# Performance work log

Hardware: AMD Instinct MI355X
Metric: run time of the kernel (lower is better)

The kernel has to match this reference:

```python
import jax, jax.numpy as jnp
import numpy as np
import math

D_MODEL = 1024
NUM_HEADS = 16
HEAD_DIM = D_MODEL // NUM_HEADS


def _sinusoidal_pe(seq_len, dim, dtype=jnp.float32):
    # Matches RotaryPositionEmbedding buffer: pe[:,0::2]=sin, pe[:,1::2]=cos
    pos = jnp.arange(seq_len, dtype=jnp.float32)[:, None]            # [S,1]
    div = jnp.exp(jnp.arange(0, dim, 2, dtype=jnp.float32) * (-math.log(10000.0) / dim))  # [dim/2]
    ang = pos * div[None, :]                                          # [S,dim/2]
    pe = jnp.stack([jnp.sin(ang), jnp.cos(ang)], axis=-1).reshape(seq_len, dim)
    return pe.astype(dtype)


def setup_inputs() -> dict:
    key = jax.random.key(0)
    ks = jax.random.split(key, 11)
    B, S, D = 4, 1024, D_MODEL
    s = 1.0 / math.sqrt(D)
    inp = {
        "q": jax.random.normal(ks[0], (B, S, D), jnp.float32),
        "k": jax.random.normal(ks[1], (B, S, D), jnp.float32),
        "v": jax.random.normal(ks[2], (B, S, D), jnp.float32),
        "Wq": jax.random.normal(ks[3], (D, D), jnp.float32) * s,
        "bq": jax.random.normal(ks[4], (D,), jnp.float32) * s,
        "Wk": jax.random.normal(ks[5], (D, D), jnp.float32) * s,
        "bk": jax.random.normal(ks[6], (D,), jnp.float32) * s,
        "Wv": jax.random.normal(ks[7], (D, D), jnp.float32) * s,
        "bv": jax.random.normal(ks[8], (D,), jnp.float32) * s,
        "Wo": jax.random.normal(ks[9], (D, D), jnp.float32) * s,
        "bo": jax.random.normal(ks[10], (D,), jnp.float32) * s,
    }
    return inp


def reference(q, k, v, Wq, bq, Wk, bk, Wv, bv, Wo, bo):
    B, S, D = q.shape
    H, hd = NUM_HEADS, HEAD_DIM
    scale = hd ** -0.5

    def proj(x, W, b):  # nn.Linear: x @ W.T + b, then [B,H,S,hd]
        return (x @ W.T + b).reshape(B, S, H, hd).transpose(0, 2, 1, 3)

    qh = proj(q, Wq, bq)
    kh = proj(k, Wk, bk)
    vh = proj(v, Wv, bv)

    pe = _sinusoidal_pe(S, hd, qh.dtype)[None, None]  # [1,1,S,hd]
    qh = qh + pe
    kh = kh + pe

    scores = jnp.einsum("bhqd,bhkd->bhqk", qh, kh) * scale  # [B,H,S,S]
    attn = jax.nn.softmax(scores, axis=-1)
    out = jnp.einsum("bhqk,bhkd->bhqd", attn, vh)            # [B,H,S,hd]
    out = out.transpose(0, 2, 1, 3).reshape(B, S, D)
    return out @ Wo.T + bo
```

## Files before the change

kernel.cpp:

```cpp
#include <hip/hip_runtime.h>
#include <hip/hip_bf16.h>

#define B_  4
#define S_  1024
#define D_  1024
#define H_  16
#define HD_ 64

typedef __bf16 bf16;
typedef __bf16 bf16x8 __attribute__((ext_vector_type(8)));
typedef __bf16 bf16x4 __attribute__((ext_vector_type(4)));
typedef float  f32x4  __attribute__((ext_vector_type(4)));

__device__ __forceinline__ void gll16(const void* g, void* l) {
    __builtin_amdgcn_global_load_lds((__attribute__((address_space(1))) void*)(void*)g,
                                     (__attribute__((address_space(3))) void*)l,
                                     16, 0, 0);
}

__global__ __launch_bounds__(256)
void convert_w_kernel(const float* __restrict__ Wq, const float* __restrict__ Wk,
                      const float* __restrict__ Wv, const float* __restrict__ Wo,
                      bf16* __restrict__ dst)
{
    const int idx   = blockIdx.x * 256 + threadIdx.x;
    const int which = idx >> 17;
    const int off   = (idx & 131071) * 8;
    const float* s  = (which == 0) ? Wq : (which == 1) ? Wk : (which == 2) ? Wv : Wo;
    const f32x4 a = *(const f32x4*)(s + off);
    const f32x4 b = *(const f32x4*)(s + off + 4);
    bf16x8 o;
#pragma unroll
    for (int jj = 0; jj < 4; ++jj) { o[jj] = (bf16)a[jj]; o[jj + 4] = (bf16)b[jj]; }
    *(bf16x8*)(dst + ((size_t)which << 20) + off) = o;
}

__global__ __launch_bounds__(256)
void qkv_proj_kernel(const float* __restrict__ qin, const float* __restrict__ kin,
                     const float* __restrict__ vin,
                     const bf16* __restrict__ Wall,
                     const float* __restrict__ bq, const float* __restrict__ bk,
                     const float* __restrict__ bv,
                     bf16* __restrict__ Qh, bf16* __restrict__ Kh,
                     bf16* __restrict__ Vt)
{
    __shared__ __align__(16) bf16 sA[128 * 32];
    __shared__ __align__(16) bf16 sB[128 * 32];

    const int z = blockIdx.z;
    const float* __restrict__ X    = (z == 0) ? qin : (z == 1) ? kin : vin;
    const float* __restrict__ bias = (z == 0) ? bq  : (z == 1) ? bk  : bv;

    const int m0   = blockIdx.y * 128;
    const int n0   = blockIdx.x * 128;
    const int tid  = threadIdx.x;
    const int lane = tid & 63;
    const int wave = tid >> 6;
    const int lr   = lane & 15;
    const int lg   = lane >> 4;
    const int mw   = (wave >> 1) * 64;
    const int nw   = (wave & 1) * 64;
    const int srow = tid >> 2;
    const int skg  = (tid & 3) * 8;

    f32x4 acc[4][4];
#pragma unroll
    for (int i = 0; i < 4; ++i)
#pragma unroll
        for (int j = 0; j < 4; ++j) acc[i][j] = (f32x4){0.f, 0.f, 0.f, 0.f};

    const float* Ab = X + (size_t)(m0 + srow) * D_ + skg;
    const bf16*  Wb = Wall + ((size_t)z << 20) + (size_t)(n0 + srow) * D_ + skg;

    for (int kt = 0; kt < 32; ++kt) {
        const int k0 = kt * 32;
        f32x4 ga[2][2];
#pragma unroll
        for (int p = 0; p < 2; ++p) {
            const float* ar = Ab + (size_t)(p * 64) * D_ + k0;
            ga[p][0] = *(const f32x4*)(ar);
            ga[p][1] = *(const f32x4*)(ar + 4);
        }
        __syncthreads();
#pragma unroll
        for (int p = 0; p < 2; ++p)
            gll16(Wb + (size_t)(p * 64) * D_ + k0, (char*)sB + p * 4096 + tid * 16);
#pragma unroll
        for (int p = 0; p < 2; ++p) {
            bf16x8 ta;
#pragma unroll
            for (int jj = 0; jj < 4; ++jj) {
                ta[jj]     = (bf16)ga[p][0][jj];
                ta[jj + 4] = (bf16)ga[p][1][jj];
            }
            *(bf16x8*)(sA + p * 2048 + tid * 8) = ta;
        }
        __syncthreads();

        bf16x8 af[4], bfr[4];
#pragma unroll
        for (int i = 0; i < 4; ++i)
            af[i] = *(const bf16x8*)(sA + (mw + 16 * i + lr) * 32 + lg * 8);
#pragma unroll
        for (int j = 0; j < 4; ++j)
            bfr[j] = *(const bf16x8*)(sB + (nw + 16 * j + lr) * 32 + lg * 8);
#pragma unroll
        for (int i = 0; i < 4; ++i)
#pragma unroll
            for (int j = 0; j < 4; ++j)
                acc[i][j] = __builtin_amdgcn_mfma_f32_16x16x32_bf16(af[i], bfr[j],
                                                                    acc[i][j], 0, 0, 0);
    }

    if (z < 2) {
        bf16* dst = (z == 0) ? Qh : Kh;
#pragma unroll
        for (int i = 0; i < 4; ++i) {
#pragma unroll
            for (int j = 0; j < 4; ++j) {
                const int n = n0 + nw + 16 * j + lr;
                const int h = n >> 6, d = n & 63;
                const float bn = bias[n];
                const float dv_rev = 0.15915494309189535f *
                    exp2f(-(float)(d & ~1) * 0.20762050593046648f);
#pragma unroll
                for (int r = 0; r < 4; ++r) {
                    const int m = m0 + mw + 16 * i + lg * 4 + r;
                    const int b = m >> 10, s = m & 1023;
                    float rev = (float)s * dv_rev;
                    rev -= floorf(rev);
                    const float sv = __builtin_amdgcn_sinf(rev);
                    const float cv = __builtin_amdgcn_cosf(rev);
                    const float pe  = (d & 1) ? cv : sv;
                    const float val = acc[i][j][r] + bn + pe;
                    dst[(size_t)((b * H_ + h) * S_ + s) * HD_ + d] = (bf16)val;
                }
            }
        }
    } else {
#pragma unroll
        for (int i = 0; i < 4; ++i) {
            const int mb = m0 + mw + 16 * i + lg * 4;
            const int b = mb >> 10, sb = mb & 1023;
#pragma unroll
            for (int j = 0; j < 4; ++j) {
                const int n = n0 + nw + 16 * j + lr;
                const int h = n >> 6, d = n & 63;
                const float bn = bias[n];
                bf16x4 pk;
#pragma unroll
                for (int r = 0; r < 4; ++r) pk[r] = (bf16)(acc[i][j][r] + bn);
                *(bf16x4*)(Vt + (size_t)((b * H_ + h) * HD_ + d) * S_ + sb) = pk;
            }
        }
    }
}

#define LDK 72
__global__ __launch_bounds__(128)
void attn_kernel(const bf16* __restrict__ Qh, const bf16* __restrict__ Kh,
                 const bf16* __restrict__ Vt, bf16* __restrict__ att)
{
    __shared__ __align__(16) bf16 sK[64 * LDK];
    __shared__ __align__(16) bf16 sV[64 * LDK];
    __shared__ __align__(16) bf16 sP[2 * 32 * LDK];

    const int tid  = threadIdx.x;
    const int lane = tid & 63;
    const int wave = tid >> 6;
    const int lr   = lane & 15;
    const int lg   = lane >> 4;
    const int bh   = blockIdx.y;
    const int qw   = blockIdx.x * 64 + wave * 32;

    const bf16* Qb = Qh + (size_t)bh * S_ * HD_;
    const bf16* Kb = Kh + (size_t)bh * S_ * HD_;
    const bf16* Vb = Vt + (size_t)bh * HD_ * S_;

    bf16x8 qa[2][2];
#pragma unroll
    for (int i = 0; i < 2; ++i)
#pragma unroll
        for (int ks = 0; ks < 2; ++ks)
            qa[i][ks] = *(const bf16x8*)(Qb + (size_t)(qw + 16 * i + lr) * HD_ +
                                         ks * 32 + lg * 8);

    f32x4 o[2][4];
    float lsum[2][4];
#pragma unroll
    for (int i = 0; i < 2; ++i) {
#pragma unroll
        for (int jd = 0; jd < 4; ++jd) o[i][jd] = (f32x4){0.f, 0.f, 0.f, 0.f};
#pragma unroll
        for (int r = 0; r < 4; ++r) lsum[i][r] = 0.f;
    }

    bf16* const pw   = sP + wave * 32 * LDK;
    const int  srow  = tid >> 3;
    const int  scol  = (tid & 7) * 8;

    for (int kc = 0; kc < 16; ++kc) {
        bf16x8 kv[4], vv[4];
#pragma unroll
        for (int p = 0; p < 4; ++p) {
            kv[p] = *(const bf16x8*)(Kb + (size_t)(kc * 64 + p * 16 + srow) * HD_ + scol);
            vv[p] = *(const bf16x8*)(Vb + (size_t)(p * 16 + srow) * S_ + kc * 64 + scol);
        }
        __syncthreads();
#pragma unroll
        for (int p = 0; p < 4; ++p) {
            *(bf16x8*)(sK + (p * 16 + srow) * LDK + scol) = kv[p];
            *(bf16x8*)(sV + (p * 16 + srow) * LDK + scol) = vv[p];
        }
        __syncthreads();

        bf16x8 kb[4][2];
#pragma unroll
        for (int jk = 0; jk < 4; ++jk)
#pragma unroll
            for (int ks = 0; ks < 2; ++ks)
                kb[jk][ks] = *(const bf16x8*)(sK + (16 * jk + lr) * LDK + ks * 32 + lg * 8);

#pragma unroll
        for (int i = 0; i < 2; ++i)
#pragma unroll
            for (int jk = 0; jk < 4; ++jk) {
                f32x4 s = (f32x4){0.f, 0.f, 0.f, 0.f};
                s = __builtin_amdgcn_mfma_f32_16x16x32_bf16(qa[i][0], kb[jk][0], s, 0, 0, 0);
                s = __builtin_amdgcn_mfma_f32_16x16x32_bf16(qa[i][1], kb[jk][1], s, 0, 0, 0);
#pragma unroll
                for (int r = 0; r < 4; ++r) {
                    const float pp = __expf(s[r] * 0.125f);
                    lsum[i][r] += pp;
                    pw[(16 * i + lg * 4 + r) * LDK + 16 * jk + lr] = (bf16)pp;
                }
            }
        asm volatile("s_waitcnt lgkmcnt(0)" ::: "memory");

#pragma unroll
        for (int ks = 0; ks < 2; ++ks) {
            bf16x8 pa[2];
#pragma unroll
            for (int i = 0; i < 2; ++i)
                pa[i] = *(const bf16x8*)(pw + (16 * i + lr) * LDK + ks * 32 + lg * 8);
#pragma unroll
            for (int jd = 0; jd < 4; ++jd) {
                const bf16x8 vb = *(const bf16x8*)(sV + (16 * jd + lr) * LDK +
                                                   ks * 32 + lg * 8);
#pragma unroll
                for (int i = 0; i < 2; ++i)
                    o[i][jd] = __builtin_amdgcn_mfma_f32_16x16x32_bf16(pa[i], vb,
                                                                       o[i][jd], 0, 0, 0);
            }
        }
    }

    const int b = bh >> 4, h = bh & 15;
#pragma unroll
    for (int i = 0; i < 2; ++i)
#pragma unroll
        for (int r = 0; r < 4; ++r) {
            float l = lsum[i][r];
#pragma unroll
            for (int off = 1; off < 16; off <<= 1)
                l += __shfl_xor(l, off, 64);
            const float inv = 1.f / l;
            const int s = qw + 16 * i + lg * 4 + r;
#pragma unroll
            for (int jd = 0; jd < 4; ++jd) {
                const int d = 16 * jd + lr;
                att[(size_t)(b * S_ + s) * D_ + h * HD_ + d] = (bf16)(o[i][jd][r] * inv);
            }
        }
}

__global__ __launch_bounds__(256)
void out_proj_kernel(const bf16* __restrict__ A, const bf16* __restrict__ Wob,
                     const float* __restrict__ bo, float* __restrict__ out)
{
    __shared__ __align__(16) bf16 sA[128 * 32];
    __shared__ __align__(16) bf16 sB[128 * 32];

    const int m0   = blockIdx.y * 128;
    const int n0   = blockIdx.x * 128;
    const int tid  = threadIdx.x;
    const int lane = tid & 63;
    const int wave = tid >> 6;
    const int lr   = lane & 15;
    const int lg   = lane >> 4;
    const int mw   = (wave >> 1) * 64;
    const int nw   = (wave & 1) * 64;
    const int srow = tid >> 2;
    const int skg  = (tid & 3) * 8;

    f32x4 acc[4][4];
#pragma unroll
    for (int i = 0; i < 4; ++i)
#pragma unroll
        for (int j = 0; j < 4; ++j) acc[i][j] = (f32x4){0.f, 0.f, 0.f, 0.f};

    const bf16* Ab = A   + (size_t)(m0 + srow) * D_ + skg;
    const bf16* Wb = Wob + (size_t)(n0 + srow) * D_ + skg;

    for (int kt = 0; kt < 32; ++kt) {
        const int k0 = kt * 32;
        __syncthreads();
#pragma unroll
        for (int p = 0; p < 2; ++p) {
            gll16(Ab + (size_t)(p * 64) * D_ + k0, (char*)sA + p * 4096 + tid * 16);
            gll16(Wb + (size_t)(p * 64) * D_ + k0, (char*)sB + p * 4096 + tid * 16);
        }
        __syncthreads();

        bf16x8 af[4], bfr[4];
#pragma unroll
        for (int i = 0; i < 4; ++i)
            af[i] = *(const bf16x8*)(sA + (mw + 16 * i + lr) * 32 + lg * 8);
#pragma unroll
        for (int j = 0; j < 4; ++j)
            bfr[j] = *(const bf16x8*)(sB + (nw + 16 * j + lr) * 32 + lg * 8);
#pragma unroll
        for (int i = 0; i < 4; ++i)
#pragma unroll
            for (int j = 0; j < 4; ++j)
                acc[i][j] = __builtin_amdgcn_mfma_f32_16x16x32_bf16(af[i], bfr[j],
                                                                    acc[i][j], 0, 0, 0);
    }

#pragma unroll
    for (int i = 0; i < 4; ++i)
#pragma unroll
        for (int j = 0; j < 4; ++j) {
            const int n = n0 + nw + 16 * j + lr;
            const float bn = bo[n];
#pragma unroll
            for (int r = 0; r < 4; ++r) {
                const int m = m0 + mw + 16 * i + lg * 4 + r;
                out[(size_t)m * D_ + n] = acc[i][j][r] + bn;
            }
        }
}

extern "C" void kernel_launch(void* const* d_in, const int* in_sizes, int n_in,
                              void* d_out, int out_size, void* d_ws, size_t ws_size,
                              hipStream_t stream)
{
    const float* q  = (const float*)d_in[0];
    const float* k  = (const float*)d_in[1];
    const float* v  = (const float*)d_in[2];
    const float* Wq = (const float*)d_in[3];
    const float* bq = (const float*)d_in[4];
    const float* Wk = (const float*)d_in[5];
    const float* bk = (const float*)d_in[6];
    const float* Wv = (const float*)d_in[7];
    const float* bv = (const float*)d_in[8];
    const float* Wo = (const float*)d_in[9];
    const float* bo = (const float*)d_in[10];

    char* ws = (char*)d_ws;
    const size_t SZ = (size_t)B_ * H_ * S_ * HD_ * sizeof(bf16);
    bf16* Qh  = (bf16*)(ws);
    bf16* Kh  = (bf16*)(ws + SZ);
    bf16* Vt  = (bf16*)(ws + 2 * SZ);
    bf16* att = (bf16*)(ws + 3 * SZ);

    bf16* Wall = (bf16*)d_out;

    convert_w_kernel<<<2048, 256, 0, stream>>>(Wq, Wk, Wv, Wo, Wall);
    qkv_proj_kernel<<<dim3(8, 32, 3), 256, 0, stream>>>(q, k, v, Wall, bq, bk, bv,
                                                        Qh, Kh, Vt);
    attn_kernel<<<dim3(16, 64), 128, 0, stream>>>(Qh, Kh, Vt, att);
    hipMemcpyAsync((void*)Qh, (const void*)(Wall + ((size_t)3 << 20)),
                   (size_t)D_ * D_ * sizeof(bf16), hipMemcpyDeviceToDevice, stream);
    out_proj_kernel<<<dim3(8, 32), 256, 0, stream>>>(att, (const bf16*)Qh, bo,
                                                     (float*)d_out);
}
```

Baseline: 233.1 us.

## Pre-convert activations to bf16 and use async LDS loads in QKV GEMM

When the workspace is large enough, one kernel converts the q/k/v activations and all four weight matrices to bf16 in scratch. The QKV projection then streams pure bf16 tiles into LDS with global_load_lds instead of converting fp32 on the fly, and the device-to-device memcpy of Wo is dropped. Grids are flattened to 1D with the m index varying fastest, so consecutive blocks share weight tiles in cache. The cost is an extra full read and write pass over the activations, and the old path is kept as a fallback for small workspaces.

```diff
diff --git a/kernel.cpp b/kernel.cpp
--- a/kernel.cpp
+++ b/kernel.cpp
@@ -16,6 +16,36 @@
     __builtin_amdgcn_global_load_lds((__attribute__((address_space(1))) void*)(void*)g,
                                      (__attribute__((address_space(3))) void*)l,
                                      16, 0, 0);
+}
+
+__global__ __launch_bounds__(256)
+void convert_all_kernel(const float* __restrict__ q, const float* __restrict__ k,
+                        const float* __restrict__ v,
+                        const float* __restrict__ Wq, const float* __restrict__ Wk,
+                        const float* __restrict__ Wv, const float* __restrict__ Wo,
+                        bf16* __restrict__ Xb, bf16* __restrict__ Wall)
+{
+    const size_t e = ((size_t)blockIdx.x * 256 + threadIdx.x) * 8;
+    const size_t M4 = (size_t)1 << 22;
+    const float* s;
+    bf16* d;
+    if (e < 3 * M4) {
+        const int which = (int)(e >> 22);
+        s = ((which == 0) ? q : (which == 1) ? k : v) + (e - ((size_t)which << 22));
+        d = Xb + e;
+    } else {
+        const size_t r = e - 3 * M4;
+        const int which = (int)(r >> 20);
+        s = ((which == 0) ? Wq : (which == 1) ? Wk : (which == 2) ? Wv : Wo) +
+            (r - ((size_t)which << 20));
+        d = Wall + r;
+    }
+    const f32x4 a = *(const f32x4*)s;
+    const f32x4 b = *(const f32x4*)(s + 4);
+    bf16x8 o;
+#pragma unroll
+    for (int jj = 0; jj < 4; ++jj) { o[jj] = (bf16)a[jj]; o[jj + 4] = (bf16)b[jj]; }
+    *(bf16x8*)d = o;
 }
 
 __global__ __launch_bounds__(256)
@@ -35,14 +65,130 @@
     *(bf16x8*)(dst + ((size_t)which << 20) + off) = o;
 }
 
+__device__ __forceinline__ void qkv_epilogue(
+    f32x4 (&acc)[4][4], int z, int m0, int n0, int mw, int nw, int lr, int lg,
+    const float* __restrict__ bias,
+    bf16* __restrict__ Qh, bf16* __restrict__ Kh, bf16* __restrict__ Vt)
+{
+    if (z < 2) {
+        bf16* dst = (z == 0) ? Qh : Kh;
+#pragma unroll
+        for (int i = 0; i < 4; ++i) {
+#pragma unroll
+            for (int j = 0; j < 4; ++j) {
+                const int n = n0 + nw + 16 * j + lr;
+                const int h = n >> 6, d = n & 63;
+                const float bn = bias[n];
+                const float dv_rev = 0.15915494309189535f *
+                    exp2f(-(float)(d & ~1) * 0.20762050593046648f);
+#pragma unroll
+                for (int r = 0; r < 4; ++r) {
+                    const int m = m0 + mw + 16 * i + lg * 4 + r;
+                    const int b = m >> 10, s = m & 1023;
+                    float rev = (float)s * dv_rev;
+                    rev -= floorf(rev);
+                    const float sv = __builtin_amdgcn_sinf(rev);
+                    const float cv = __builtin_amdgcn_cosf(rev);
+                    const float pe  = (d & 1) ? cv : sv;
+                    const float val = acc[i][j][r] + bn + pe;
+                    dst[(size_t)((b * H_ + h) * S_ + s) * HD_ + d] = (bf16)val;
+                }
+            }
+        }
+    } else {
+#pragma unroll
+        for (int i = 0; i < 4; ++i) {
+            const int mb = m0 + mw + 16 * i + lg * 4;
+            const int b = mb >> 10, sb = mb & 1023;
+#pragma unroll
+            for (int j = 0; j < 4; ++j) {
+                const int n = n0 + nw + 16 * j + lr;
+                const int h = n >> 6, d = n & 63;
+                const float bn = bias[n];
+                bf16x4 pk;
+#pragma unroll
+                for (int r = 0; r < 4; ++r) pk[r] = (bf16)(acc[i][j][r] + bn);
+                *(bf16x4*)(Vt + (size_t)((b * H_ + h) * HD_ + d) * S_ + sb) = pk;
+            }
+        }
+    }
+}
+
 __global__ __launch_bounds__(256)
-void qkv_proj_kernel(const float* __restrict__ qin, const float* __restrict__ kin,
-                     const float* __restrict__ vin,
-                     const bf16* __restrict__ Wall,
-                     const float* __restrict__ bq, const float* __restrict__ bk,
-                     const float* __restrict__ bv,
-                     bf16* __restrict__ Qh, bf16* __restrict__ Kh,
-                     bf16* __restrict__ Vt)
+void qkv_proj_bf16_kernel(const bf16* __restrict__ Xb, const bf16* __restrict__ Wall,
+                          const float* __restrict__ bq, const float* __restrict__ bk,
+                          const float* __restrict__ bv,
+                          bf16* __restrict__ Qh, bf16* __restrict__ Kh,
+                          bf16* __restrict__ Vt)
+{
+    __shared__ __align__(16) bf16 sA[128 * 32];
+    __shared__ __align__(16) bf16 sB[128 * 32];
+
+    const int blk  = blockIdx.x;
+    const int mIdx = blk & 31;
+    const int t    = blk >> 5;
+    const int nIdx = t & 7;
+    const int z    = t >> 3;
+
+    const int m0 = mIdx * 128, n0 = nIdx * 128;
+    const bf16* __restrict__ X = Xb + ((size_t)z << 22);
+    const bf16* __restrict__ W = Wall + ((size_t)z << 20);
+    const float* __restrict__ bias = (z == 0) ? bq : (z == 1) ? bk : bv;
+
+    const int tid  = threadIdx.x;
+    const int lane = tid & 63;
+    const int wave = tid >> 6;
+    const int lr   = lane & 15;
+    const int lg   = lane >> 4;
+    const int mw   = (wave >> 1) * 64;
+    const int nw   = (wave & 1) * 64;
+    const int srow = tid >> 2;
+    const int skg  = (tid & 3) * 8;
+
+    f32x4 acc[4][4];
+#pragma unroll
+    for (int i = 0; i < 4; ++i)
+#pragma unroll
+        for (int j = 0; j < 4; ++j) acc[i][j] = (f32x4){0.f, 0.f, 0.f, 0.f};
+
+    const bf16* Ab = X + (size_t)(m0 + srow) * D_ + skg;
+    const bf16* Wb = W + (size_t)(n0 + srow) * D_ + skg;
+
+    for (int kt = 0; kt < 32; ++kt) {
+        const int k0 = kt * 32;
+        __syncthreads();
+#pragma unroll
+        for (int p = 0; p < 2; ++p) {
+            gll16(Ab + (size_t)(p * 64) * D_ + k0, (char*)sA + p * 4096 + tid * 16);
+            gll16(Wb + (size_t)(p * 64) * D_ + k0, (char*)sB + p * 4096 + tid * 16);
+        }
+        __syncthreads();
+
+        bf16x8 af[4], bfr[4];
+#pragma unroll
+        for (int i = 0; i < 4; ++i)
+            af[i] = *(const bf16x8*)(sA + (mw + 16 * i + lr) * 32 + lg * 8);
+#pragma unroll
+        for (int j = 0; j < 4; ++j)
+            bfr[j] = *(const bf16x8*)(sB + (nw + 16 * j + lr) * 32 + lg * 8);
+#pragma unroll
+        for (int i = 0; i < 4; ++i)
+#pragma unroll
+            for (int j = 0; j < 4; ++j)
+                acc[i][j] = __builtin_amdgcn_mfma_f32_16x16x32_bf16(af[i], bfr[j],
+                                                                    acc[i][j], 0, 0, 0);
+    }
+    qkv_epilogue(acc, z, m0, n0, mw, nw, lr, lg, bias, Qh, Kh, Vt);
+}
+
+__global__ __launch_bounds__(256)
+void qkv_proj_mixed_kernel(const float* __restrict__ qin, const float* __restrict__ kin,
+                           const float* __restrict__ vin,
+                           const bf16* __restrict__ Wall,
+                           const float* __restrict__ bq, const float* __restrict__ bk,
+                           const float* __restrict__ bv,
+                           bf16* __restrict__ Qh, bf16* __restrict__ Kh,
+                           bf16* __restrict__ Vt)
 {
     __shared__ __align__(16) bf16 sA[128 * 32];
     __shared__ __align__(16) bf16 sB[128 * 32];
@@ -111,49 +257,7 @@
                 acc[i][j] = __builtin_amdgcn_mfma_f32_16x16x32_bf16(af[i], bfr[j],
                                                                     acc[i][j], 0, 0, 0);
     }
-
-    if (z < 2) {
-        bf16* dst = (z == 0) ? Qh : Kh;
-#pragma unroll
-        for (int i = 0; i < 4; ++i) {
-#pragma unroll
-            for (int j = 0; j < 4; ++j) {
-                const int n = n0 + nw + 16 * j + lr;
-                const int h = n >> 6, d = n & 63;
-                const float bn = bias[n];
-                const float dv_rev = 0.15915494309189535f *
-                    exp2f(-(float)(d & ~1) * 0.20762050593046648f);
-#pragma unroll
-                for (int r = 0; r < 4; ++r) {
-                    const int m = m0 + mw + 16 * i + lg * 4 + r;
-                    const int b = m >> 10, s = m & 1023;
-                    float rev = (float)s * dv_rev;
-                    rev -= floorf(rev);
-                    const float sv = __builtin_amdgcn_sinf(rev);
-                    const float cv = __builtin_amdgcn_cosf(rev);
-                    const float pe  = (d & 1) ? cv : sv;
-                    const float val = acc[i][j][r] + bn + pe;
-                    dst[(size_t)((b * H_ + h) * S_ + s) * HD_ + d] = (bf16)val;
-                }
-            }
-        }
-    } else {
-#pragma unroll
-        for (int i = 0; i < 4; ++i) {
-            const int mb = m0 + mw + 16 * i + lg * 4;
-            const int b = mb >> 10, sb = mb & 1023;
-#pragma unroll
-            for (int j = 0; j < 4; ++j) {
-                const int n = n0 + nw + 16 * j + lr;
-                const int h = n >> 6, d = n & 63;
-                const float bn = bias[n];
-                bf16x4 pk;
-#pragma unroll
-                for (int r = 0; r < 4; ++r) pk[r] = (bf16)(acc[i][j][r] + bn);
-                *(bf16x4*)(Vt + (size_t)((b * H_ + h) * HD_ + d) * S_ + sb) = pk;
-            }
-        }
-    }
+    qkv_epilogue(acc, z, m0, n0, mw, nw, lr, lg, bias, Qh, Kh, Vt);
 }
 
 #define LDK 72
@@ -170,8 +274,9 @@
     const int wave = tid >> 6;
     const int lr   = lane & 15;
     const int lg   = lane >> 4;
-    const int bh   = blockIdx.y;
-    const int qw   = blockIdx.x * 64 + wave * 32;
+    const int bh   = blockIdx.x & 63;
+    const int qt   = blockIdx.x >> 6;
+    const int qw   = qt * 64 + wave * 32;
 
     const bf16* Qb = Qh + (size_t)bh * S_ * HD_;
     const bf16* Kb = Kh + (size_t)bh * S_ * HD_;
@@ -281,8 +386,11 @@
     __shared__ __align__(16) bf16 sA[128 * 32];
     __shared__ __align__(16) bf16 sB[128 * 32];
 
-    const int m0   = blockIdx.y * 128;
-    const int n0   = blockIdx.x * 128;
+    const int blk  = blockIdx.x;
+    const int mIdx = blk & 31;
+    const int nIdx = blk >> 5;
+    const int m0 = mIdx * 128, n0 = nIdx * 128;
+
     const int tid  = threadIdx.x;
     const int lane = tid & 63;
     const int wave = tid >> 6;
@@ -358,20 +466,32 @@
     const float* bo = (const float*)d_in[10];
 
     char* ws = (char*)d_ws;
-    const size_t SZ = (size_t)B_ * H_ * S_ * HD_ * sizeof(bf16);
+    const size_t MB8 = (size_t)8 * 1024 * 1024;
     bf16* Qh  = (bf16*)(ws);
-    bf16* Kh  = (bf16*)(ws + SZ);
-    bf16* Vt  = (bf16*)(ws + 2 * SZ);
-    bf16* att = (bf16*)(ws + 3 * SZ);
-
-    bf16* Wall = (bf16*)d_out;
-
-    convert_w_kernel<<<2048, 256, 0, stream>>>(Wq, Wk, Wv, Wo, Wall);
-    qkv_proj_kernel<<<dim3(8, 32, 3), 256, 0, stream>>>(q, k, v, Wall, bq, bk, bv,
-                                                        Qh, Kh, Vt);
-    attn_kernel<<<dim3(16, 64), 128, 0, stream>>>(Qh, Kh, Vt, att);
-    hipMemcpyAsync((void*)Qh, (const void*)(Wall + ((size_t)3 << 20)),
-                   (size_t)D_ * D_ * sizeof(bf16), hipMemcpyDeviceToDevice, stream);
-    out_proj_kernel<<<dim3(8, 32), 256, 0, stream>>>(att, (const bf16*)Qh, bo,
-                                                     (float*)d_out);
-}
+    bf16* Kh  = (bf16*)(ws + MB8);
+    bf16* Vt  = (bf16*)(ws + 2 * MB8);
+    bf16* att = (bf16*)(ws + 3 * MB8);
+
+    if (ws_size >= (size_t)64 * 1024 * 1024) {
+        bf16* Xb   = (bf16*)(ws + 4 * MB8);
+        bf16* Wall = (bf16*)(ws + 7 * MB8);
+        convert_all_kernel<<<8192, 256, 0, stream>>>(q, k, v, Wq, Wk, Wv, Wo,
+                                                     Xb, Wall);
+        qkv_proj_bf16_kernel<<<768, 256, 0, stream>>>(Xb, Wall, bq, bk, bv,
+                                                      Qh, Kh, Vt);
+        attn_kernel<<<1024, 128, 0, stream>>>(Qh, Kh, Vt, att);
+        out_proj_kernel<<<256, 256, 0, stream>>>(att, Wall + ((size_t)3 << 20),
+                                                 bo, (float*)d_out);
+    } else {
+        bf16* Wall = (bf16*)d_out;
+        convert_w_kernel<<<2048, 256, 0, stream>>>(Wq, Wk, Wv, Wo, Wall);
+        qkv_proj_mixed_kernel<<<dim3(8, 32, 3), 256, 0, stream>>>(
+            q, k, v, Wall, bq, bk, bv, Qh, Kh, Vt);
+        attn_kernel<<<1024, 128, 0, stream>>>(Qh, Kh, Vt, att);
+        hipMemcpyAsync((void*)Qh, (const void*)(Wall + ((size_t)3 << 20)),
+                       (size_t)D_ * D_ * sizeof(bf16), hipMemcpyDeviceToDevice,
+                       stream);
+        out_proj_kernel<<<256, 256, 0, stream>>>(att, (const bf16*)Qh, bo,
+                                                 (float*)d_out);
+    }
+}
```

Result: faster. 213.5 us (-8.4%).
